# Performance work log

Measured on AMD Instinct MI355X. Metric: run time of the kernel, lower is better.

Reference implementation:

```python
import jax, jax.numpy as jnp
import numpy as np

N_NEURONS, D_MODEL, D_FF, N_PATTERNS, K_PATTERNS = 2048, 1024, 4096, 64, 4
B, S, K = 4, 2048, 8


def setup_inputs() -> dict:
    key = jax.random.key(0)
    ks = jax.random.split(key, 10)
    return {
        "x": jax.random.normal(ks[0], (B, S, D_MODEL), jnp.float32),
        "router_out": jax.random.normal(ks[1], (B, S, D_MODEL), jnp.float32),
        "topk_neuron_idx": jax.random.randint(ks[2], (B, S, K), 0, N_NEURONS),
        "topk_neuron_weights": jax.random.uniform(ks[3], (B, S, K), jnp.float32),
        "selected_neurons": jax.random.normal(ks[4], (B, S, K, D_MODEL), jnp.float32),
        "pattern_queries": jax.random.normal(ks[5], (N_PATTERNS, D_MODEL), jnp.float32) * 0.02,
        "gates": jax.random.normal(ks[6], (N_PATTERNS, D_FF), jnp.float32) * 0.02,
        "up_w": jax.random.normal(ks[7], (D_FF, D_MODEL), jnp.float32) / np.sqrt(D_MODEL),
        "up_b": jnp.zeros((D_FF,), jnp.float32),
        "down_w": jax.random.normal(ks[8], (D_MODEL, D_FF), jnp.float32) / np.sqrt(D_FF),
        "down_b": jnp.zeros((D_MODEL,), jnp.float32),
    }


def reference(x, router_out, topk_neuron_idx, topk_neuron_weights, selected_neurons,
              pattern_queries, gates, up_w, up_b, down_w, down_b):
    D = selected_neurons.shape[-1]
    # pattern scoring: [P, B, S, K]
    sim = jnp.einsum('pd,bskd->pbsk', pattern_queries, selected_neurons) / jnp.sqrt(jnp.float32(D))
    pattern_scores = jnp.einsum('pbsk,bsk->bsp', sim, topk_neuron_weights)  # weighted sum over K, permuted
    topk_scores, topk_pattern_idx = jax.lax.top_k(pattern_scores, K_PATTERNS)  # [B,S,k]
    topk_pattern_weights = jax.nn.softmax(topk_scores, axis=-1)
    selected_gates = gates[topk_pattern_idx]  # [B,S,k,d_ff]
    ffn_gate = jnp.einsum('bsk,bskf->bsf', topk_pattern_weights, selected_gates)
    h = jnp.einsum('bsd,fd->bsf', x, up_w) + up_b
    h = jax.nn.gelu(h * jax.nn.sigmoid(ffn_gate), approximate=False)
    return jnp.einsum('bsf,df->bsd', h, down_w) + down_b
```

## Files before the change

kernel.cpp:

```cpp
#include <hip/hip_runtime.h>
#include <hip/hip_bf16.h>
#include <math.h>

#define R_   8192
#define DM   1024
#define DFF  4096
#define NP   64
#define KN   8

typedef __bf16 bf16x8 __attribute__((ext_vector_type(8)));
typedef float  f32x4  __attribute__((ext_vector_type(4)));

__device__ __forceinline__ unsigned short f2bf(float f) {
  union { float f; unsigned u; } v; v.f = f;
  unsigned u = v.u;
  return (unsigned short)((u + 0x7FFFu + ((u >> 16) & 1u)) >> 16);
}

__device__ __forceinline__ float dot4(const float4 a, const float4 b) {
  return a.x * b.x + a.y * b.y + a.z * b.z + a.w * b.w;
}

__device__ __forceinline__ void fma4(float4& a, float w, const float4 s) {
  a.x += w * s.x; a.y += w * s.y; a.z += w * s.z; a.w += w * s.w;
}

__global__ __launch_bounds__(256) void cvt_bf16_kernel(
    const float* __restrict__ in, unsigned short* __restrict__ out, int n8) {
  int i = blockIdx.x * 256 + threadIdx.x;
  if (i >= n8) return;
  const float4* p = (const float4*)in + (size_t)i * 2;
  float4 a = p[0], b = p[1];
  uint4 r;
  r.x = (unsigned)f2bf(a.x) | ((unsigned)f2bf(a.y) << 16);
  r.y = (unsigned)f2bf(a.z) | ((unsigned)f2bf(a.w) << 16);
  r.z = (unsigned)f2bf(b.x) | ((unsigned)f2bf(b.y) << 16);
  r.w = (unsigned)f2bf(b.z) | ((unsigned)f2bf(b.w) << 16);
  ((uint4*)out)[i] = r;
}

__global__ __launch_bounds__(256) void vcomp_kernel(
    const float* __restrict__ sn,
    const float* __restrict__ tw,
    float* __restrict__ v)
{
  const int r = blockIdx.x;
  const int t = threadIdx.x;
  float w[KN];
#pragma unroll
  for (int k = 0; k < KN; ++k) w[k] = tw[(size_t)r * KN + k];
  const float* base = sn + (size_t)r * (KN * DM) + t * 4;
  float4 a = {0.f, 0.f, 0.f, 0.f};
#pragma unroll
  for (int k = 0; k < KN; ++k) fma4(a, w[k], *(const float4*)(base + k * DM));
  *(float4*)(v + (size_t)r * DM + t * 4) = a;
}

__global__ __launch_bounds__(256, 2) void score_kernel(
    const float* __restrict__ v,
    const float* __restrict__ pq,
    int*   __restrict__ out_idx,
    float* __restrict__ out_w)
{
  const int lane = threadIdx.x & 63;
  const int wave = threadIdx.x >> 6;
  const int pos0 = (blockIdx.x * 4 + wave) * 4;

  float4 vr[4][4];
#pragma unroll
  for (int p = 0; p < 4; ++p) {
    const float4* s = (const float4*)(v + (size_t)(pos0 + p) * DM + lane * 16);
    vr[p][0] = s[0]; vr[p][1] = s[1]; vr[p][2] = s[2]; vr[p][3] = s[3];
  }

  float sreg[4];
#pragma unroll 1
  for (int pat = 0; pat < NP; ++pat) {
    const float4* q = (const float4*)(pq + pat * DM + lane * 16);
    const float4 q0 = q[0], q1 = q[1], q2 = q[2], q3 = q[3];
    float part[4];
#pragma unroll
    for (int p = 0; p < 4; ++p)
      part[p] = dot4(q0, vr[p][0]) + dot4(q1, vr[p][1]) +
                dot4(q2, vr[p][2]) + dot4(q3, vr[p][3]);
#pragma unroll
    for (int off = 32; off >= 1; off >>= 1) {
#pragma unroll
      for (int p = 0; p < 4; ++p)
        part[p] += __shfl_xor(part[p], off, 64);
    }
    if (lane == pat) {
#pragma unroll
      for (int p = 0; p < 4; ++p) sreg[p] = part[p] * 0.03125f;
    }
  }

#pragma unroll
  for (int p = 0; p < 4; ++p) {
    float cur = sreg[p];
    float m0, m1, m2, m3; int i0, i1, i2, i3;
#define ARGMAX_STEP(MV, MI)                                   \
    {                                                         \
      float bv = cur; int bi = lane;                          \
      _Pragma("unroll")                                       \
      for (int off = 32; off >= 1; off >>= 1) {               \
        float ov = __shfl_xor(bv, off, 64);                   \
        int   oi = __shfl_xor(bi, off, 64);                   \
        if (ov > bv || (ov == bv && oi < bi)) { bv = ov; bi = oi; } \
      }                                                       \
      MV = bv; MI = bi;                                       \
      if (lane == bi) cur = -3.0e38f;                         \
    }
    ARGMAX_STEP(m0, i0) ARGMAX_STEP(m1, i1) ARGMAX_STEP(m2, i2) ARGMAX_STEP(m3, i3)
#undef ARGMAX_STEP
    const float e1 = __expf(m1 - m0), e2 = __expf(m2 - m0), e3 = __expf(m3 - m0);
    const float inv = 1.f / (1.f + e1 + e2 + e3);
    if (lane < 4) {
      const int r = pos0 + p;
      const int myi = (lane == 0) ? i0 : (lane == 1) ? i1 : (lane == 2) ? i2 : i3;
      const float mye = (lane == 0) ? 1.f : (lane == 1) ? e1 : (lane == 2) ? e2 : e3;
      out_idx[r * 4 + lane] = myi;
      out_w[r * 4 + lane] = mye * inv;
    }
  }
}

__device__ __forceinline__ void gll16(const void* g, void* l) {
  __builtin_amdgcn_global_load_lds(
      (const __attribute__((address_space(1))) unsigned int*)g,
      (__attribute__((address_space(3))) unsigned int*)l, 16, 0, 0);
}

template <int K, int N, int BM, int BN, int WM, int WN, int RING, int MODE>
__global__ __launch_bounds__(512, 2) void gemm_kernel(
    const unsigned short* __restrict__ A,
    const unsigned short* __restrict__ Bm,
    const float* __restrict__ bias,
    const int*   __restrict__ pidx,
    const float* __restrict__ pwt,
    const float* __restrict__ gates,
    void* __restrict__ Cout)
{
  extern __shared__ char smem[];
  constexpr int NT     = K / 32;
  constexpr int MF     = WM / 16;
  constexpr int NF     = WN / 16;
  constexpr int NWC    = BN / WN;
  constexpr int LA     = BM / 128;
  constexpr int LB     = BN / 128;
  constexpr int KEEP   = (RING - 3) * (LA + LB);
  constexpr int TILE_A = BM * 64;
  constexpr int TILE   = TILE_A + BN * 64;
  constexpr int NBN    = N / BN;

  const int tid  = threadIdx.x;
  const int lane = tid & 63;
  const int wid  = tid >> 6;
  const int wr   = wid / NWC;
  const int wc   = wid % NWC;

  const int grid = gridDim.x;
  const int cpx  = grid >> 3;
  const int swz  = (blockIdx.x & 7) * cpx + (blockIdx.x >> 3);
  const int brow = swz / NBN;
  const int bcol = swz % NBN;

  const unsigned short* Ab = A  + (size_t)brow * BM * K;
  const unsigned short* Bb = Bm + (size_t)bcol * BN * K;

  int aoffE[LA], boffE[LB];
#pragma unroll
  for (int i = 0; i < LA; ++i)
    aoffE[i] = (i * 128 + wid * 16 + (lane >> 2)) * K + (lane & 3) * 8;
#pragma unroll
  for (int i = 0; i < LB; ++i)
    boffE[i] = (i * 128 + wid * 16 + (lane >> 2)) * K + (lane & 3) * 8;

  const int ard = (wr * WM + (lane & 15)) * 64 + (lane >> 4) * 16;
  const int brd = (wc * WN + (lane & 15)) * 64 + (lane >> 4) * 16;

  f32x4 acc[MF][NF];
#pragma unroll
  for (int m = 0; m < MF; ++m)
#pragma unroll
    for (int n = 0; n < NF; ++n)
      acc[m][n] = (f32x4){0.f, 0.f, 0.f, 0.f};

  bf16x8 fa0[MF], fb0[NF], fa1[MF], fb1[NF];

  for (int t = 0; t < RING - 1; ++t) {
    const int kE = t * 32;
    char* sba = smem + t * TILE;
#pragma unroll
    for (int i = 0; i < LA; ++i)
      gll16(Ab + kE + aoffE[i], sba + i * 8192 + wid * 1024);
#pragma unroll
    for (int i = 0; i < LB; ++i)
      gll16(Bb + kE + boffE[i], sba + TILE_A + i * 8192 + wid * 1024);
  }
  asm volatile("s_waitcnt vmcnt(%0)" ::"i"(KEEP) : "memory");
  __builtin_amdgcn_s_barrier();
  {
    const char* abase = smem + ard;
    const char* bbase = smem + TILE_A + brd;
#pragma unroll
    for (int m = 0; m < MF; ++m) fa0[m] = *(const bf16x8*)(abase + m * 1024);
#pragma unroll
    for (int n = 0; n < NF; ++n) fb0[n] = *(const bf16x8*)(bbase + n * 1024);
  }
  int rb = 1, sb = RING - 1;

#define GITER(S, FAC, FBC, FAN, FBN)                                          \
  {                                                                           \
    if ((S) + 1 < NT) {                                                       \
      const char* abase = smem + rb * TILE + ard;                             \
      const char* bbase = smem + rb * TILE + TILE_A + brd;                    \
      _Pragma("unroll") for (int m = 0; m < MF; ++m)                          \
        FAN[m] = *(const bf16x8*)(abase + m * 1024);                          \
      _Pragma("unroll") for (int n = 0; n < NF; ++n)                          \
        FBN[n] = *(const bf16x8*)(bbase + n * 1024);                          \
    }                                                                         \
    if ((S) + RING - 1 < NT) {                                                \
      const int kE = ((S) + RING - 1) * 32;                                   \
      char* sba = smem + sb * TILE;                                           \
      _Pragma("unroll") for (int i = 0; i < LA; ++i)                          \
        gll16(Ab + kE + aoffE[i], sba + i * 8192 + wid * 1024);               \
      _Pragma("unroll") for (int i = 0; i < LB; ++i)                          \
        gll16(Bb + kE + boffE[i], sba + TILE_A + i * 8192 + wid * 1024);      \
      asm volatile("s_waitcnt vmcnt(%0)" ::"i"(KEEP) : "memory");             \
    } else {                                                                  \
      asm volatile("s_waitcnt vmcnt(0)" ::: "memory");                        \
    }                                                                         \
    __builtin_amdgcn_s_barrier();                                             \
    __builtin_amdgcn_s_setprio(1);                                            \
    _Pragma("unroll") for (int m = 0; m < MF; ++m)                            \
      _Pragma("unroll") for (int n = 0; n < NF; ++n)                          \
        acc[m][n] = __builtin_amdgcn_mfma_f32_16x16x32_bf16(                  \
            FAC[m], FBC[n], acc[m][n], 0, 0, 0);                              \
    __builtin_amdgcn_s_setprio(0);                                            \
    __builtin_amdgcn_s_barrier();                                             \
    rb = rb + 1 == RING ? 0 : rb + 1;                                         \
    sb = sb + 1 == RING ? 0 : sb + 1;                                         \
  }

  for (int s = 0; s < NT; s += 2) {
    GITER(s, fa0, fb0, fa1, fb1);
    GITER(s + 1, fa1, fb1, fa0, fb0);
  }
#undef GITER

  const int crow0 = brow * BM + wr * WM;
  const int ccol0 = bcol * BN + wc * WN + (lane & 15);
  const int rsub  = (lane >> 4) * 4;

  if (MODE == 0) {
    unsigned short* H = (unsigned short*)Cout;
#pragma unroll
    for (int m = 0; m < MF; ++m) {
      const int rbase = crow0 + m * 16 + rsub;
      int   ia[4][4];
      float wa[4][4];
#pragma unroll
      for (int j = 0; j < 4; ++j) {
        const int4   iq = *(const int4*)(pidx + (size_t)(rbase + j) * 4);
        const float4 wq = *(const float4*)(pwt + (size_t)(rbase + j) * 4);
        ia[j][0] = iq.x; ia[j][1] = iq.y; ia[j][2] = iq.z; ia[j][3] = iq.w;
        wa[j][0] = wq.x; wa[j][1] = wq.y; wa[j][2] = wq.z; wa[j][3] = wq.w;
      }
#pragma unroll
      for (int n = 0; n < NF; ++n) {
        const int col = ccol0 + n * 16;
        const float ub = bias[col];
#pragma unroll
        for (int j = 0; j < 4; ++j) {
          float g = wa[j][0] * gates[(size_t)ia[j][0] * DFF + col]
                  + wa[j][1] * gates[(size_t)ia[j][1] * DFF + col]
                  + wa[j][2] * gates[(size_t)ia[j][2] * DFF + col]
                  + wa[j][3] * gates[(size_t)ia[j][3] * DFF + col];
          const float u   = acc[m][n][j] + ub;
          const float val = u * (1.f / (1.f + __expf(-g)));
          const float h   = 0.5f * val * (1.f + erff(val * 0.70710678118654752f));
          H[(size_t)(rbase + j) * N + col] = f2bf(h);
        }
      }
    }
  } else {
    float* O = (float*)Cout;
#pragma unroll
    for (int m = 0; m < MF; ++m) {
      const int rbase = crow0 + m * 16 + rsub;
#pragma unroll
      for (int n = 0; n < NF; ++n) {
        const int col = ccol0 + n * 16;
        const float db = bias[col];
#pragma unroll
        for (int j = 0; j < 4; ++j)
          O[(size_t)(rbase + j) * N + col] = acc[m][n][j] + db;
      }
    }
  }
}

extern "C" void kernel_launch(void* const* d_in, const int* in_sizes, int n_in,
                              void* d_out, int out_size, void* d_ws, size_t ws_size,
                              hipStream_t stream) {
  const float* x     = (const float*)d_in[0];
  const float* tw    = (const float*)d_in[3];
  const float* sn    = (const float*)d_in[4];
  const float* pq    = (const float*)d_in[5];
  const float* gates = (const float*)d_in[6];
  const float* upw   = (const float*)d_in[7];
  const float* upb   = (const float*)d_in[8];
  const float* dnw   = (const float*)d_in[9];
  const float* dnb   = (const float*)d_in[10];
  float* out = (float*)d_out;

  char* p = (char*)d_ws;
  unsigned short* xb  = (unsigned short*)p; p += (size_t)R_ * DM * 2;
  unsigned short* uwb = (unsigned short*)p; p += (size_t)DFF * DM * 2;
  unsigned short* dwb = (unsigned short*)p; p += (size_t)DM * DFF * 2;
  unsigned short* H   = (unsigned short*)p; p += (size_t)R_ * DFF * 2;
  int*   pidx = (int*)p;   p += (size_t)R_ * 4 * sizeof(int);
  float* pwt  = (float*)p; p += (size_t)R_ * 4 * sizeof(float);
  float* vbuf = (float*)p; p += (size_t)R_ * DM * sizeof(float);

  cvt_bf16_kernel<<<(R_ * DM / 8) / 256, 256, 0, stream>>>(x, xb, R_ * DM / 8);
  cvt_bf16_kernel<<<(DFF * DM / 8) / 256, 256, 0, stream>>>(upw, uwb, DFF * DM / 8);
  cvt_bf16_kernel<<<(DM * DFF / 8) / 256, 256, 0, stream>>>(dnw, dwb, DM * DFF / 8);

  vcomp_kernel<<<R_, 256, 0, stream>>>(sn, tw, vbuf);
  score_kernel<<<R_ / 16, 256, 0, stream>>>(vbuf, pq, pidx, pwt);

  auto* k1 = gemm_kernel<DM, DFF, 256, 256, 128, 64, 4, 0>;
  auto* k2 = gemm_kernel<DFF, DM, 256, 128, 64, 64, 6, 1>;
  hipFuncSetAttribute((const void*)k1, hipFuncAttributeMaxDynamicSharedMemorySize,
                      4 * (256 + 256) * 64);
  hipFuncSetAttribute((const void*)k2, hipFuncAttributeMaxDynamicSharedMemorySize,
                      6 * (256 + 128) * 64);

  k1<<<(R_ / 256) * (DFF / 256), 512, 4 * (256 + 256) * 64, stream>>>(
      xb, uwb, upb, pidx, pwt, gates, (void*)H);
  k2<<<(R_ / 256) * (DM / 128), 512, 6 * (256 + 128) * 64, stream>>>(
      H, dwb, dnb, nullptr, nullptr, nullptr, (void*)out);
}
```

Measured before the change: 377.8 us.

## Swizzle LDS layout and restructure GEMM pipeline to fixed 4-slot ring

Applies an XOR swizzle to the k-chunk position used when global-to-LDS loads fill each row and when fragments are read back, aiming to remove LDS bank conflicts on fragment reads. The main loop is unrolled by four with compile-time ring slots, replacing the runtime ring-index arithmetic. The next stage's global loads are now issued before the wait and barrier, and fragment reads move after the barrier. The second GEMM's ring shrinks from six to four stages, which lowers LDS use but shortens its prefetch depth.

```diff
diff --git a/kernel.cpp b/kernel.cpp
--- a/kernel.cpp
+++ b/kernel.cpp
@@ -131,7 +131,7 @@
       (__attribute__((address_space(3))) unsigned int*)l, 16, 0, 0);
 }
 
-template <int K, int N, int BM, int BN, int WM, int WN, int RING, int MODE>
+template <int K, int N, int BM, int BN, int WM, int WN, int MODE>
 __global__ __launch_bounds__(512, 2) void gemm_kernel(
     const unsigned short* __restrict__ A,
     const unsigned short* __restrict__ Bm,
@@ -148,7 +148,8 @@
   constexpr int NWC    = BN / WN;
   constexpr int LA     = BM / 128;
   constexpr int LB     = BN / 128;
-  constexpr int KEEP   = (RING - 3) * (LA + LB);
+  constexpr int KEEPM  = 2 * (LA + LB);
+  constexpr int KEEP1  = (LA + LB);
   constexpr int TILE_A = BM * 64;
   constexpr int TILE   = TILE_A + BN * 64;
   constexpr int NBN    = N / BN;
@@ -161,23 +162,25 @@
 
   const int grid = gridDim.x;
   const int cpx  = grid >> 3;
-  const int swz  = (blockIdx.x & 7) * cpx + (blockIdx.x >> 3);
-  const int brow = swz / NBN;
-  const int bcol = swz % NBN;
+  const int swzb = (blockIdx.x & 7) * cpx + (blockIdx.x >> 3);
+  const int brow = swzb / NBN;
+  const int bcol = swzb % NBN;
 
   const unsigned short* Ab = A  + (size_t)brow * BM * K;
   const unsigned short* Bb = Bm + (size_t)bcol * BN * K;
 
+  const int sswz = ((lane & 3) ^ ((lane >> 3) & 3)) * 8;
   int aoffE[LA], boffE[LB];
 #pragma unroll
   for (int i = 0; i < LA; ++i)
-    aoffE[i] = (i * 128 + wid * 16 + (lane >> 2)) * K + (lane & 3) * 8;
+    aoffE[i] = (i * 128 + wid * 16 + (lane >> 2)) * K + sswz;
 #pragma unroll
   for (int i = 0; i < LB; ++i)
-    boffE[i] = (i * 128 + wid * 16 + (lane >> 2)) * K + (lane & 3) * 8;
-
-  const int ard = (wr * WM + (lane & 15)) * 64 + (lane >> 4) * 16;
-  const int brd = (wc * WN + (lane & 15)) * 64 + (lane >> 4) * 16;
+    boffE[i] = (i * 128 + wid * 16 + (lane >> 2)) * K + sswz;
+
+  const int rswz = ((lane >> 4) ^ ((lane >> 1) & 3)) * 16;
+  const int ard  = (wr * WM + (lane & 15)) * 64 + rswz;
+  const int brd  = (wc * WN + (lane & 15)) * 64 + rswz;
 
   f32x4 acc[MF][NF];
 #pragma unroll
@@ -188,66 +191,62 @@
 
   bf16x8 fa0[MF], fb0[NF], fa1[MF], fb1[NF];
 
-  for (int t = 0; t < RING - 1; ++t) {
-    const int kE = t * 32;
-    char* sba = smem + t * TILE;
-#pragma unroll
-    for (int i = 0; i < LA; ++i)
-      gll16(Ab + kE + aoffE[i], sba + i * 8192 + wid * 1024);
-#pragma unroll
-    for (int i = 0; i < LB; ++i)
-      gll16(Bb + kE + boffE[i], sba + TILE_A + i * 8192 + wid * 1024);
-  }
-  asm volatile("s_waitcnt vmcnt(%0)" ::"i"(KEEP) : "memory");
+#define STAGE(S, SB)                                                        \
+  {                                                                         \
+    const int kE = (S) * 32;                                                \
+    char* sba = smem + (SB) * TILE;                                         \
+    _Pragma("unroll") for (int i = 0; i < LA; ++i)                          \
+      gll16(Ab + kE + aoffE[i], sba + i * 8192 + wid * 1024);               \
+    _Pragma("unroll") for (int i = 0; i < LB; ++i)                          \
+      gll16(Bb + kE + boffE[i], sba + TILE_A + i * 8192 + wid * 1024);      \
+  }
+
+  STAGE(0, 0) STAGE(1, 1) STAGE(2, 2)
+  asm volatile("s_waitcnt vmcnt(%0)" ::"i"(KEEPM) : "memory");
   __builtin_amdgcn_s_barrier();
   {
-    const char* abase = smem + ard;
-    const char* bbase = smem + TILE_A + brd;
-#pragma unroll
-    for (int m = 0; m < MF; ++m) fa0[m] = *(const bf16x8*)(abase + m * 1024);
-#pragma unroll
-    for (int n = 0; n < NF; ++n) fb0[n] = *(const bf16x8*)(bbase + n * 1024);
-  }
-  int rb = 1, sb = RING - 1;
-
-#define GITER(S, FAC, FBC, FAN, FBN)                                          \
-  {                                                                           \
-    if ((S) + 1 < NT) {                                                       \
-      const char* abase = smem + rb * TILE + ard;                             \
-      const char* bbase = smem + rb * TILE + TILE_A + brd;                    \
-      _Pragma("unroll") for (int m = 0; m < MF; ++m)                          \
-        FAN[m] = *(const bf16x8*)(abase + m * 1024);                          \
-      _Pragma("unroll") for (int n = 0; n < NF; ++n)                          \
-        FBN[n] = *(const bf16x8*)(bbase + n * 1024);                          \
-    }                                                                         \
-    if ((S) + RING - 1 < NT) {                                                \
-      const int kE = ((S) + RING - 1) * 32;                                   \
-      char* sba = smem + sb * TILE;                                           \
-      _Pragma("unroll") for (int i = 0; i < LA; ++i)                          \
-        gll16(Ab + kE + aoffE[i], sba + i * 8192 + wid * 1024);               \
-      _Pragma("unroll") for (int i = 0; i < LB; ++i)                          \
-        gll16(Bb + kE + boffE[i], sba + TILE_A + i * 8192 + wid * 1024);      \
-      asm volatile("s_waitcnt vmcnt(%0)" ::"i"(KEEP) : "memory");             \
-    } else {                                                                  \
-      asm volatile("s_waitcnt vmcnt(0)" ::: "memory");                        \
-    }                                                                         \
-    __builtin_amdgcn_s_barrier();                                             \
-    __builtin_amdgcn_s_setprio(1);                                            \
-    _Pragma("unroll") for (int m = 0; m < MF; ++m)                            \
-      _Pragma("unroll") for (int n = 0; n < NF; ++n)                          \
-        acc[m][n] = __builtin_amdgcn_mfma_f32_16x16x32_bf16(                  \
-            FAC[m], FBC[n], acc[m][n], 0, 0, 0);                              \
-    __builtin_amdgcn_s_setprio(0);                                            \
-    __builtin_amdgcn_s_barrier();                                             \
-    rb = rb + 1 == RING ? 0 : rb + 1;                                         \
-    sb = sb + 1 == RING ? 0 : sb + 1;                                         \
-  }
-
-  for (int s = 0; s < NT; s += 2) {
-    GITER(s, fa0, fb0, fa1, fb1);
-    GITER(s + 1, fa1, fb1, fa0, fb0);
-  }
+    const char* ab = smem + ard;
+    const char* bb = smem + TILE_A + brd;
+#pragma unroll
+    for (int m = 0; m < MF; ++m) fa0[m] = *(const bf16x8*)(ab + m * 1024);
+#pragma unroll
+    for (int n = 0; n < NF; ++n) fb0[n] = *(const bf16x8*)(bb + n * 1024);
+  }
+
+#define GITER(S, RB, SB, DOSTAGE, KEEPV, DOREAD, FAC, FBC, FAN, FBN)        \
+  {                                                                         \
+    if (DOSTAGE) STAGE((S) + 3, SB)                                         \
+    asm volatile("s_waitcnt vmcnt(%0)" ::"i"(KEEPV) : "memory");            \
+    __builtin_amdgcn_s_barrier();                                           \
+    if (DOREAD) {                                                           \
+      const char* ab = smem + (RB) * TILE + ard;                            \
+      const char* bb = smem + (RB) * TILE + TILE_A + brd;                   \
+      _Pragma("unroll") for (int m = 0; m < MF; ++m)                        \
+        FAN[m] = *(const bf16x8*)(ab + m * 1024);                           \
+      _Pragma("unroll") for (int n = 0; n < NF; ++n)                        \
+        FBN[n] = *(const bf16x8*)(bb + n * 1024);                           \
+    }                                                                       \
+    __builtin_amdgcn_s_setprio(1);                                          \
+    _Pragma("unroll") for (int m = 0; m < MF; ++m)                          \
+      _Pragma("unroll") for (int n = 0; n < NF; ++n)                        \
+        acc[m][n] = __builtin_amdgcn_mfma_f32_16x16x32_bf16(                \
+            FAC[m], FBC[n], acc[m][n], 0, 0, 0);                            \
+    __builtin_amdgcn_s_setprio(0);                                          \
+    __builtin_amdgcn_s_barrier();                                           \
+  }
+
+  for (int s = 0; s < NT - 4; s += 4) {
+    GITER(s + 0, 1, 3, 1, KEEPM, 1, fa0, fb0, fa1, fb1)
+    GITER(s + 1, 2, 0, 1, KEEPM, 1, fa1, fb1, fa0, fb0)
+    GITER(s + 2, 3, 1, 1, KEEPM, 1, fa0, fb0, fa1, fb1)
+    GITER(s + 3, 0, 2, 1, KEEPM, 1, fa1, fb1, fa0, fb0)
+  }
+  GITER(NT - 4, 1, 3, 1, KEEPM, 1, fa0, fb0, fa1, fb1)
+  GITER(NT - 3, 2, 0, 0, KEEP1, 1, fa1, fb1, fa0, fb0)
+  GITER(NT - 2, 3, 1, 0, 0,     1, fa0, fb0, fa1, fb1)
+  GITER(NT - 1, 0, 2, 0, 0,     0, fa1, fb1, fa0, fb0)
 #undef GITER
+#undef STAGE
 
   const int crow0 = brow * BM + wr * WM;
   const int ccol0 = bcol * BN + wc * WN + (lane & 15);
@@ -331,15 +330,15 @@
   vcomp_kernel<<<R_, 256, 0, stream>>>(sn, tw, vbuf);
   score_kernel<<<R_ / 16, 256, 0, stream>>>(vbuf, pq, pidx, pwt);
 
-  auto* k1 = gemm_kernel<DM, DFF, 256, 256, 128, 64, 4, 0>;
-  auto* k2 = gemm_kernel<DFF, DM, 256, 128, 64, 64, 6, 1>;
+  auto* k1 = gemm_kernel<DM, DFF, 256, 256, 128, 64, 0>;
+  auto* k2 = gemm_kernel<DFF, DM, 256, 128, 64, 64, 1>;
   hipFuncSetAttribute((const void*)k1, hipFuncAttributeMaxDynamicSharedMemorySize,
                       4 * (256 + 256) * 64);
   hipFuncSetAttribute((const void*)k2, hipFuncAttributeMaxDynamicSharedMemorySize,
-                      6 * (256 + 128) * 64);
+                      4 * (256 + 128) * 64);
 
   k1<<<(R_ / 256) * (DFF / 256), 512, 4 * (256 + 256) * 64, stream>>>(
       xb, uwb, upb, pidx, pwt, gates, (void*)H);
-  k2<<<(R_ / 256) * (DM / 128), 512, 6 * (256 + 128) * 64, stream>>>(
+  k2<<<(R_ / 256) * (DM / 128), 512, 4 * (256 + 128) * 64, stream>>>(
       H, dwb, dnb, nullptr, nullptr, nullptr, (void*)out);
 }
```

Result: faster. 368.0 us (-2.6%).
